# Optimization experiments

Measured on AMD Instinct MI355X. Metric: run time of the kernel, lower is better.

The kernel has to match this reference:

```python
import jax, jax.numpy as jnp
import numpy as np

D_MODEL = 1024
HIDDEN = 4096
NUM_EXPERTS = 8
TOP_K = 2
N_TOKENS = 4 * 2048  # batch * seq


def setup_inputs() -> dict:
    key = jax.random.key(0)
    k_x, k_w, k_i, k1, k2, k3 = jax.random.split(key, 6)
    x = jax.random.normal(k_x, (4, 2048, D_MODEL), dtype=jnp.float32)
    expert_weights = jax.random.uniform(k_w, (N_TOKENS, TOP_K), dtype=jnp.float32)
    expert_indices = jax.random.randint(k_i, (N_TOKENS, TOP_K), 0, NUM_EXPERTS)
    scale = 1.0 / np.sqrt(D_MODEL)
    w1 = jax.random.normal(k1, (NUM_EXPERTS, D_MODEL, HIDDEN), dtype=jnp.float32) * scale
    w3 = jax.random.normal(k3, (NUM_EXPERTS, D_MODEL, HIDDEN), dtype=jnp.float32) * scale
    w2 = jax.random.normal(k2, (NUM_EXPERTS, HIDDEN, D_MODEL), dtype=jnp.float32) * (1.0 / np.sqrt(HIDDEN))
    return {"x": x, "expert_weights": expert_weights, "expert_indices": expert_indices,
            "w1": w1, "w2": w2, "w3": w3}


def reference(x, expert_weights, expert_indices, w1, w2, w3):
    # forward_once of ParallelDroplessMLP (single-rank dropless MoE).
    in_shape = x.shape
    d_model = x.shape[-1]
    num_experts = w1.shape[0]
    xf = x.reshape(-1, d_model)                        # (N, d)
    top_k = expert_weights.shape[-1]
    ew = expert_weights.reshape(-1)                    # (N*top_k,)
    ei = expert_indices.reshape(-1).astype(jnp.int32)  # (N*top_k,)

    # indices_and_bins: stable sort by expert id + histogram
    order = jnp.argsort(ei)                            # (T,) permuted row -> flat (token, k) slot
    tokens_per_expert = jnp.bincount(ei, length=num_experts).astype(jnp.int32)

    # gather: replicate each token top_k times, grouped by expert
    token_of_row = order // top_k                      # (T,)
    xg = jnp.take(xf, token_of_row, axis=0)            # (T, d)

    # grouped GEMM (MegaBlocks-style) SwiGLU per expert via ragged_dot
    h = jax.nn.silu(jax.lax.ragged_dot(xg, w1, tokens_per_expert)) \
        * jax.lax.ragged_dot(xg, w3, tokens_per_expert)            # (T, hidden)
    y = jax.lax.ragged_dot(h, w2, tokens_per_expert)               # (T, d)

    # scatter: weighted un-permute back to token positions
    y = y * ew[order][:, None]
    out = jnp.zeros_like(xf).at[token_of_row].add(y)
    return out.reshape(in_shape), tokens_per_expert
```

## Files before the change

### kernel.cpp

```cpp
#include <hip/hip_runtime.h>

#define NTOK 8192
#define TROWS 16384
#define DM 1024
#define HID 4096
#define NEXP 8
#define MAXT256 72
#define MAXT128 136

typedef __bf16 bf16x8 __attribute__((ext_vector_type(8)));
typedef float  f32x4  __attribute__((ext_vector_type(4)));
typedef short  s16x4  __attribute__((ext_vector_type(4)));

#define BAR() do { asm volatile("" ::: "memory"); __builtin_amdgcn_s_barrier(); asm volatile("" ::: "memory"); } while(0)
#define VM6() asm volatile("s_waitcnt vmcnt(6)" ::: "memory")
#define VM0() asm volatile("s_waitcnt vmcnt(0)" ::: "memory")
#define VM8() asm volatile("s_waitcnt vmcnt(8)" ::: "memory")

__device__ __forceinline__ short f2bf(float f) {
  union { float f; unsigned u; } v; v.f = f;
  unsigned r = (v.u + 0x7fffu + ((v.u >> 16) & 1u)) >> 16;
  return (short)r;
}
__device__ __forceinline__ float bf2f(short s) {
  union { unsigned u; float f; } z; z.u = ((unsigned)(unsigned short)s) << 16; return z.f;
}

__device__ __forceinline__ void gload16(const short* g, short* l) {
  __builtin_amdgcn_global_load_lds(
      (const __attribute__((address_space(1))) void*)g,
      (__attribute__((address_space(3))) void*)l, 16, 0, 0);
}

__global__ void k_meta(const int* __restrict__ ei, int* __restrict__ meta,
                       float* __restrict__ outCounts) {
  __shared__ int c[NEXP];
  int tid = threadIdx.x;
  if (tid < NEXP) c[tid] = 0;
  __syncthreads();
  for (int i = tid; i < TROWS; i += 256) atomicAdd(&c[ei[i]], 1);
  __syncthreads();
  if (tid == 0) {
    int off = 0, s = 0, s2 = 0;
    for (int e = 0; e < NEXP; ++e) {
      int ce = c[e];
      meta[e] = ce;
      meta[8 + e] = off;
      meta[16 + e] = off;
      outCounts[e] = (float)ce;
      for (int r0 = 0; r0 < ce; r0 += 256) {
        meta[32 + 3*s] = e; meta[32 + 3*s + 1] = off + r0;
        meta[32 + 3*s + 2] = (ce - r0 < 256) ? (ce - r0) : 256; ++s;
      }
      for (int r0 = 0; r0 < ce; r0 += 128) {
        meta[256 + 3*s2] = e; meta[256 + 3*s2 + 1] = off + r0;
        meta[256 + 3*s2 + 2] = (ce - r0 < 128) ? (ce - r0) : 128; ++s2;
      }
      off += ce;
    }
    for (; s < MAXT256; ++s)  { meta[32 + 3*s] = 0;  meta[32 + 3*s + 1] = 0;  meta[32 + 3*s + 2] = 0; }
    for (; s2 < MAXT128; ++s2){ meta[256 + 3*s2] = 0; meta[256 + 3*s2 + 1] = 0; meta[256 + 3*s2 + 2] = 0; }
  }
}

__global__ void k_scatter(const int* __restrict__ ei, int* __restrict__ meta,
                          int* __restrict__ rowmap, int* __restrict__ inv) {
  int t = blockIdx.x * blockDim.x + threadIdx.x;
  if (t < TROWS) {
    int e = ei[t];
    int p = atomicAdd(&meta[16 + e], 1);
    rowmap[p] = t;
    inv[t] = p;
  }
}

__global__ void k_transpose64(const float* __restrict__ in, short* __restrict__ out,
                              int R, int C) {
  __shared__ short lt[64][68];
  int e = blockIdx.z;
  int c0 = blockIdx.x * 64, r0 = blockIdx.y * 64;
  int t = threadIdx.x;
  int rr = t >> 4, cc = (t & 15) * 4;
  const float* src = in + ((size_t)e * R + r0 + rr) * C + c0 + cc;
#pragma unroll
  for (int i = 0; i < 4; ++i) {
    f32x4 v = *(const f32x4*)(src + (size_t)i * 16 * C);
#pragma unroll
    for (int j = 0; j < 4; ++j) lt[cc + j][rr + i*16] = f2bf(v[j]);
  }
  __syncthreads();
  int c2 = t >> 4, r4 = (t & 15) * 4;
  short* dst = out + ((size_t)e * C + c0 + c2) * R + r0 + r4;
#pragma unroll
  for (int i = 0; i < 4; ++i) {
    s16x4 o = *(const s16x4*)&lt[c2 + i*16][r4];
    *(s16x4*)(dst + (size_t)i * 16 * R) = o;
  }
}

__global__ void k_cvt_x(const float* __restrict__ x, short* __restrict__ xb) {
  const int n4 = NTOK * DM / 4;
  for (int i = blockIdx.x * blockDim.x + threadIdx.x; i < n4; i += gridDim.x * blockDim.x) {
    f32x4 v = ((const f32x4*)x)[i];
    s16x4 s = { f2bf(v.x), f2bf(v.y), f2bf(v.z), f2bf(v.w) };
    ((s16x4*)xb)[i] = s;
  }
}

__global__ __launch_bounds__(512, 2) void k_gemm1(
    const short* __restrict__ xb, const short* __restrict__ w1t, const short* __restrict__ w3t,
    const int* __restrict__ rowmap, const int* __restrict__ meta, short* __restrict__ hbuf) {
  int bid = blockIdx.x;
  int swz = (bid & 7) * 288 + (bid >> 3);
  int slot = swz % MAXT256;
  int bn   = swz / MAXT256;
  int rows = meta[32 + 3*slot + 2];
  if (rows <= 0) return;
  int e    = meta[32 + 3*slot];
  int row0 = meta[32 + 3*slot + 1];

  __shared__ short lA [2][256 * 64];
  __shared__ short lB1[2][128 * 64];
  __shared__ short lB3[2][128 * 64];

  int tid = threadIdx.x, l = tid & 63, w = tid >> 6;
  int wr = (w >> 2) * 128, wc = (w & 3) * 32;
  int lr = l & 15, cb = (l >> 4) * 16, axor = (lr & 7) << 4;
  int srow = l >> 3;
  int scol = ((l & 7) ^ srow) * 8;

  const short* aG[2][2];
#pragma unroll
  for (int h = 0; h < 2; ++h)
#pragma unroll
    for (int i = 0; i < 2; ++i) {
      int r = h*128 + w*16 + i*8 + srow;
      int rc = r < rows ? r : rows - 1;
      int tok = rowmap[row0 + rc] >> 1;
      aG[h][i] = xb + (size_t)tok * DM + scol;
    }
  const short *b1G[2], *b3G[2];
#pragma unroll
  for (int i = 0; i < 2; ++i) {
    size_t grow = (size_t)e * HID + (size_t)bn * 128 + w*16 + i*8 + srow;
    b1G[i] = w1t + grow * DM + scol;
    b3G[i] = w3t + grow * DM + scol;
  }

  f32x4 acc1[2][4][2], acc3[2][4][2];
#pragma unroll
  for (int h = 0; h < 2; ++h)
#pragma unroll
    for (int i = 0; i < 4; ++i)
#pragma unroll
      for (int j = 0; j < 2; ++j) {
        acc1[h][i][j] = (f32x4){0.f,0.f,0.f,0.f};
        acc3[h][i][j] = (f32x4){0.f,0.f,0.f,0.f};
      }

  auto stgA = [&](int buf, int h, int kt) {
    gload16(aG[h][0] + kt, &lA[buf][(h*128 + w*16    ) * 64]);
    gload16(aG[h][1] + kt, &lA[buf][(h*128 + w*16 + 8) * 64]);
  };
  auto stgB1 = [&](int buf, int kt) {
    gload16(b1G[0] + kt, &lB1[buf][(w*16    ) * 64]);
    gload16(b1G[1] + kt, &lB1[buf][(w*16 + 8) * 64]);
  };
  auto stgB3 = [&](int buf, int kt) {
    gload16(b3G[0] + kt, &lB3[buf][(w*16    ) * 64]);
    gload16(b3G[1] + kt, &lB3[buf][(w*16 + 8) * 64]);
  };

  stgA(0, 0, 0); stgA(0, 1, 0); stgB1(0, 0); stgB3(0, 0);
  stgB1(1, 64); stgB3(1, 64); stgA(1, 0, 64);
  VM6();
  BAR();

  const int NT = DM / 64;
  int c = 0;
  for (int t = 0; t < NT; ++t, c ^= 1) {
    int kn  = t*64 + 64;
    int kn2 = t*64 + 128;
    const char* cA  = (const char*)&lA [c][0];
    const char* cB1 = (const char*)&lB1[c][0];
    const char* cB3 = (const char*)&lB3[c][0];

    bf16x8 alo[4][2], b1w[2][2];
#pragma unroll
    for (int i = 0; i < 4; ++i)
#pragma unroll
      for (int kk = 0; kk < 2; ++kk)
        alo[i][kk] = *(const bf16x8*)(cA + (wr + i*16 + lr)*128 + ((kk*64 + cb) ^ axor));
#pragma unroll
    for (int j = 0; j < 2; ++j)
#pragma unroll
      for (int kk = 0; kk < 2; ++kk)
        b1w[j][kk] = *(const bf16x8*)(cB1 + (wc + j*16 + lr)*128 + ((kk*64 + cb) ^ axor));
    if (t + 1 < NT) stgA(c ^ 1, 1, kn);
    BAR();
    __builtin_amdgcn_s_setprio(1);
#pragma unroll
    for (int i = 0; i < 4; ++i)
#pragma unroll
      for (int j = 0; j < 2; ++j)
#pragma unroll
        for (int kk = 0; kk < 2; ++kk)
          acc1[0][i][j] = __builtin_amdgcn_mfma_f32_16x16x32_bf16(alo[i][kk], b1w[j][kk], acc1[0][i][j], 0, 0, 0);
    __builtin_amdgcn_s_setprio(0);
    BAR();

    bf16x8 b3w[2][2];
#pragma unroll
    for (int j = 0; j < 2; ++j)
#pragma unroll
      for (int kk = 0; kk < 2; ++kk)
        b3w[j][kk] = *(const bf16x8*)(cB3 + (wc + j*16 + lr)*128 + ((kk*64 + cb) ^ axor));
    if (t + 2 < NT) stgB1(c, kn2);
    BAR();
    __builtin_amdgcn_s_setprio(1);
#pragma unroll
    for (int i = 0; i < 4; ++i)
#pragma unroll
      for (int j = 0; j < 2; ++j)
#pragma unroll
        for (int kk = 0; kk < 2; ++kk)
          acc3[0][i][j] = __builtin_amdgcn_mfma_f32_16x16x32_bf16(alo[i][kk], b3w[j][kk], acc3[0][i][j], 0, 0, 0);
    __builtin_amdgcn_s_setprio(0);
    BAR();

    bf16x8 ahi[4][2];
#pragma unroll
    for (int i = 0; i < 4; ++i)
#pragma unroll
      for (int kk = 0; kk < 2; ++kk)
        ahi[i][kk] = *(const bf16x8*)(cA + (wr + 64 + i*16 + lr)*128 + ((kk*64 + cb) ^ axor));
    if (t + 2 < NT) stgB3(c, kn2);
    BAR();
    __builtin_amdgcn_s_setprio(1);
#pragma unroll
    for (int i = 0; i < 4; ++i)
#pragma unroll
      for (int j = 0; j < 2; ++j)
#pragma unroll
        for (int kk = 0; kk < 2; ++kk)
          acc1[1][i][j] = __builtin_amdgcn_mfma_f32_16x16x32_bf16(ahi[i][kk], b1w[j][kk], acc1[1][i][j], 0, 0, 0);
    __builtin_amdgcn_s_setprio(0);
    BAR();

    if (t + 2 < NT) stgA(c, 0, kn2);
    __builtin_amdgcn_s_setprio(1);
#pragma unroll
    for (int i = 0; i < 4; ++i)
#pragma unroll
      for (int j = 0; j < 2; ++j)
#pragma unroll
        for (int kk = 0; kk < 2; ++kk)
          acc3[1][i][j] = __builtin_amdgcn_mfma_f32_16x16x32_bf16(ahi[i][kk], b3w[j][kk], acc3[1][i][j], 0, 0, 0);
    __builtin_amdgcn_s_setprio(0);
    if (t < NT - 2) { VM6(); } else { VM0(); }
    BAR();
  }

#pragma unroll
  for (int h = 0; h < 2; ++h)
#pragma unroll
    for (int i = 0; i < 4; ++i)
#pragma unroll
      for (int q = 0; q < 4; ++q) {
        int r = wr + h*64 + i*16 + (l >> 4)*4 + q;
        if (r < rows) {
          size_t base = (size_t)(row0 + r) * HID + (size_t)bn * 128 + wc;
#pragma unroll
          for (int j = 0; j < 2; ++j) {
            float g = acc1[h][i][j][q], u3 = acc3[h][i][j][q];
            float sv = g / (1.f + __expf(-g));
            hbuf[base + j*16 + lr] = f2bf(sv * u3);
          }
        }
      }
}

__global__ __launch_bounds__(256) void k_gemm2(
    const short* __restrict__ hbuf, const short* __restrict__ w2t,
    const int* __restrict__ meta, short* __restrict__ y) {
  int bid = blockIdx.x;
  int swz = (bid & 7) * (MAXT128 * 8 / 8) + (bid >> 3);
  int slot = swz % MAXT128;
  int bn   = swz / MAXT128;
  int rows = meta[256 + 3*slot + 2];
  if (rows <= 0) return;
  int e    = meta[256 + 3*slot];
  int row0 = meta[256 + 3*slot + 1];

  __shared__ short lA[2][128 * 64];
  __shared__ short lB[2][128 * 64];

  int tid = threadIdx.x;
  int l = tid & 63, w = tid >> 6;

  int srow = w*8 + (l >> 3);
  int scol = ((l & 7) ^ (l >> 3)) * 8;

  const short* aG[4];
  for (int p = 0; p < 4; ++p) {
    int r = p*32 + srow;
    int rc = r < rows ? r : rows - 1;
    aG[p] = hbuf + (size_t)(row0 + rc) * HID + scol;
  }
  const short* bG[4];
  for (int p = 0; p < 4; ++p) {
    size_t grow = (size_t)e * DM + (size_t)bn * 128 + p*32 + srow;
    bG[p] = w2t + grow * HID + scol;
  }

  f32x4 acc[4][4];
  for (int i = 0; i < 4; ++i)
    for (int j = 0; j < 4; ++j) acc[i][j] = (f32x4){0.f, 0.f, 0.f, 0.f};

  int wr = (w >> 1) * 64, wc = (w & 1) * 64;
  int lr = l & 15;
  int cb = (l >> 4) * 16;
  int axor = (lr & 7) << 4;

  auto stage = [&](int buf, int kt) {
#pragma unroll
    for (int p = 0; p < 4; ++p) {
      gload16(aG[p] + kt, &lA[buf][(p*32 + w*8) * 64]);
      gload16(bG[p] + kt, &lB[buf][(p*32 + w*8) * 64]);
    }
  };
  auto compute = [&](int cur) {
    const char* cA = (const char*)&lA[cur][0];
    const char* cB = (const char*)&lB[cur][0];
    __builtin_amdgcn_s_setprio(1);
#pragma unroll
    for (int kk2 = 0; kk2 < 2; ++kk2) {
      int co = (kk2*64 + cb) ^ axor;
      bf16x8 a[4], b[4];
#pragma unroll
      for (int i = 0; i < 4; ++i) a[i] = *(const bf16x8*)(cA + (wr + i*16 + lr)*128 + co);
#pragma unroll
      for (int j = 0; j < 4; ++j) b[j] = *(const bf16x8*)(cB + (wc + j*16 + lr)*128 + co);
#pragma unroll
      for (int i = 0; i < 4; ++i)
#pragma unroll
        for (int j = 0; j < 4; ++j)
          acc[i][j] = __builtin_amdgcn_mfma_f32_16x16x32_bf16(a[i], b[j], acc[i][j], 0, 0, 0);
    }
    __builtin_amdgcn_s_setprio(0);
  };

  stage(0, 0);
  int cur = 0;
  for (int kt = 64; kt <= HID; kt += 64) {
    if (kt < HID) {
      stage(cur ^ 1, kt);
      VM8();
    } else {
      VM0();
    }
    __builtin_amdgcn_s_barrier();
    compute(cur);
    asm volatile("" ::: "memory");
    __builtin_amdgcn_s_barrier();
    cur ^= 1;
  }

  for (int i = 0; i < 4; ++i)
    for (int q = 0; q < 4; ++q) {
      int r = wr + i*16 + (l >> 4)*4 + q;
      if (r < rows) {
        size_t obase = (size_t)(row0 + r) * DM + (size_t)bn * 128 + wc;
        for (int j = 0; j < 4; ++j)
          y[obase + j*16 + lr] = f2bf(acc[i][j][q]);
      }
    }
}

__global__ void k_unperm(const short* __restrict__ y, const int* __restrict__ inv,
                         const float* __restrict__ ew, float* __restrict__ out) {
  int i = blockIdx.x * 256 + threadIdx.x;
  int tok = i >> 8, c = i & 255;
  int p0 = inv[2*tok], p1 = inv[2*tok + 1];
  float w0 = ew[2*tok], w1v = ew[2*tok + 1];
  s16x4 a = ((const s16x4*)y)[(size_t)p0 * 256 + c];
  s16x4 b = ((const s16x4*)y)[(size_t)p1 * 256 + c];
  f32x4 r;
#pragma unroll
  for (int j = 0; j < 4; ++j) r[j] = w0 * bf2f(a[j]) + w1v * bf2f(b[j]);
  ((f32x4*)out)[i] = r;
}

extern "C" void kernel_launch(void* const* d_in, const int* in_sizes, int n_in,
                              void* d_out, int out_size, void* d_ws, size_t ws_size,
                              hipStream_t stream) {
  const float* x  = (const float*)d_in[0];
  const float* ew = (const float*)d_in[1];
  const int*   ei = (const int*)d_in[2];
  const float* w1 = (const float*)d_in[3];
  const float* w2 = (const float*)d_in[4];
  const float* w3 = (const float*)d_in[5];
  float* out = (float*)d_out;
  char*  ws  = (char*)d_ws;

  short* w1t = (short*)(ws + 0);
  short* w3t = (short*)(ws + 67108864);
  short* w2t = (short*)(ws + 134217728);
  short* xb  = (short*)(ws + 201326592);
  short* hb  = (short*)(ws + 218103808);
  int*   meta   = (int*)(ws + 352321536);
  int*   rowmap = (int*)(ws + 352321536 + 8192);
  int*   inv    = (int*)(ws + 352321536 + 73728);
  short* y      = (short*)(ws + 0);

  k_meta<<<1, 256, 0, stream>>>(ei, meta, out + (size_t)NTOK * DM);
  k_scatter<<<TROWS / 256, 256, 0, stream>>>(ei, meta, rowmap, inv);
  k_transpose64<<<dim3(HID/64, DM/64, NEXP), 256, 0, stream>>>(w1, w1t, DM, HID);
  k_transpose64<<<dim3(HID/64, DM/64, NEXP), 256, 0, stream>>>(w3, w3t, DM, HID);
  k_transpose64<<<dim3(DM/64, HID/64, NEXP), 256, 0, stream>>>(w2, w2t, HID, DM);
  k_cvt_x<<<2048, 256, 0, stream>>>(x, xb);
  k_gemm1<<<MAXT256 * (HID/128), 512, 0, stream>>>(xb, w1t, w3t, rowmap, meta, hb);
  k_gemm2<<<MAXT128 * (DM/128), 256, 0, stream>>>(hb, w2t, meta, y);
  k_unperm<<<NTOK * DM / 4 / 256, 256, 0, stream>>>(y, inv, ew, out);
}
```

Before: 801.9 us.

## Software-pipeline gemm2 into quadrant phases with finer-grained LDS prefetch

Restructures the second grouped GEMM's K loop into four quadrant MFMA phases, each issuing a portion of the next tile's global-to-LDS loads and synchronising with barriers, so loads are spread across compute instead of issued in one burst per tile. It also reworks the weight transpose kernel to stage fp32 values in a padded LDS tile and convert to bf16 on the read side. The finer interleaving aims to hide memory latency in gemm2, at the cost of more barriers per K step and more intricate buffer-reuse ordering.

```diff
diff --git a/kernel.cpp b/kernel.cpp
--- a/kernel.cpp
+++ b/kernel.cpp
@@ -15,7 +15,6 @@
 #define BAR() do { asm volatile("" ::: "memory"); __builtin_amdgcn_s_barrier(); asm volatile("" ::: "memory"); } while(0)
 #define VM6() asm volatile("s_waitcnt vmcnt(6)" ::: "memory")
 #define VM0() asm volatile("s_waitcnt vmcnt(0)" ::: "memory")
-#define VM8() asm volatile("s_waitcnt vmcnt(8)" ::: "memory")
 
 __device__ __forceinline__ short f2bf(float f) {
   union { float f; unsigned u; } v; v.f = f;
@@ -76,24 +75,23 @@
 
 __global__ void k_transpose64(const float* __restrict__ in, short* __restrict__ out,
                               int R, int C) {
-  __shared__ short lt[64][68];
+  __shared__ float lt[64][65];
   int e = blockIdx.z;
   int c0 = blockIdx.x * 64, r0 = blockIdx.y * 64;
   int t = threadIdx.x;
   int rr = t >> 4, cc = (t & 15) * 4;
   const float* src = in + ((size_t)e * R + r0 + rr) * C + c0 + cc;
 #pragma unroll
+  for (int i = 0; i < 4; ++i)
+    *(f32x4*)&lt[rr + i*16][cc] = *(const f32x4*)(src + (size_t)i * 16 * C);
+  __syncthreads();
+  int cN = t >> 4, r4 = (t & 15) * 4;
+  short* dst = out + ((size_t)e * C + c0 + cN) * R + r0 + r4;
+#pragma unroll
   for (int i = 0; i < 4; ++i) {
-    f32x4 v = *(const f32x4*)(src + (size_t)i * 16 * C);
-#pragma unroll
-    for (int j = 0; j < 4; ++j) lt[cc + j][rr + i*16] = f2bf(v[j]);
-  }
-  __syncthreads();
-  int c2 = t >> 4, r4 = (t & 15) * 4;
-  short* dst = out + ((size_t)e * C + c0 + c2) * R + r0 + r4;
-#pragma unroll
-  for (int i = 0; i < 4; ++i) {
-    s16x4 o = *(const s16x4*)&lt[c2 + i*16][r4];
+    s16x4 o;
+#pragma unroll
+    for (int j = 0; j < 4; ++j) o[j] = f2bf(lt[r4 + j][cN + i*16]);
     *(s16x4*)(dst + (size_t)i * 16 * R) = o;
   }
 }
@@ -284,7 +282,7 @@
     const short* __restrict__ hbuf, const short* __restrict__ w2t,
     const int* __restrict__ meta, short* __restrict__ y) {
   int bid = blockIdx.x;
-  int swz = (bid & 7) * (MAXT128 * 8 / 8) + (bid >> 3);
+  int swz = (bid & 7) * 136 + (bid >> 3);
   int slot = swz % MAXT128;
   int bn   = swz / MAXT128;
   int rows = meta[256 + 3*slot + 2];
@@ -295,82 +293,138 @@
   __shared__ short lA[2][128 * 64];
   __shared__ short lB[2][128 * 64];
 
-  int tid = threadIdx.x;
-  int l = tid & 63, w = tid >> 6;
-
-  int srow = w*8 + (l >> 3);
-  int scol = ((l & 7) ^ (l >> 3)) * 8;
+  int tid = threadIdx.x, l = tid & 63, w = tid >> 6;
+  int wr = (w >> 1) * 64, wc = (w & 1) * 64;
+  int lr = l & 15, cb = (l >> 4) * 16, axor = (lr & 7) << 4;
+  int srow = l >> 3;
+  int scol = ((l & 7) ^ srow) * 8;
 
   const short* aG[4];
-  for (int p = 0; p < 4; ++p) {
-    int r = p*32 + srow;
+#pragma unroll
+  for (int g = 0; g < 4; ++g) {
+    int r = g*32 + w*8 + srow;
     int rc = r < rows ? r : rows - 1;
-    aG[p] = hbuf + (size_t)(row0 + rc) * HID + scol;
+    aG[g] = hbuf + (size_t)(row0 + rc) * HID + scol;
   }
   const short* bG[4];
-  for (int p = 0; p < 4; ++p) {
-    size_t grow = (size_t)e * DM + (size_t)bn * 128 + p*32 + srow;
-    bG[p] = w2t + grow * HID + scol;
+#pragma unroll
+  for (int g = 0; g < 4; ++g) {
+    size_t grow = (size_t)e * DM + (size_t)bn * 128 + g*32 + w*8 + srow;
+    bG[g] = w2t + grow * HID + scol;
   }
 
   f32x4 acc[4][4];
+#pragma unroll
   for (int i = 0; i < 4; ++i)
-    for (int j = 0; j < 4; ++j) acc[i][j] = (f32x4){0.f, 0.f, 0.f, 0.f};
-
-  int wr = (w >> 1) * 64, wc = (w & 1) * 64;
-  int lr = l & 15;
-  int cb = (l >> 4) * 16;
-  int axor = (lr & 7) << 4;
-
-  auto stage = [&](int buf, int kt) {
-#pragma unroll
-    for (int p = 0; p < 4; ++p) {
-      gload16(aG[p] + kt, &lA[buf][(p*32 + w*8) * 64]);
-      gload16(bG[p] + kt, &lB[buf][(p*32 + w*8) * 64]);
-    }
+#pragma unroll
+    for (int j = 0; j < 4; ++j) acc[i][j] = (f32x4){0.f,0.f,0.f,0.f};
+
+  auto stgA = [&](int buf, int g, int kt) {
+    gload16(aG[g] + kt, &lA[buf][(g*32 + w*8) * 64]);
   };
-  auto compute = [&](int cur) {
-    const char* cA = (const char*)&lA[cur][0];
-    const char* cB = (const char*)&lB[cur][0];
-    __builtin_amdgcn_s_setprio(1);
-#pragma unroll
-    for (int kk2 = 0; kk2 < 2; ++kk2) {
-      int co = (kk2*64 + cb) ^ axor;
-      bf16x8 a[4], b[4];
-#pragma unroll
-      for (int i = 0; i < 4; ++i) a[i] = *(const bf16x8*)(cA + (wr + i*16 + lr)*128 + co);
-#pragma unroll
-      for (int j = 0; j < 4; ++j) b[j] = *(const bf16x8*)(cB + (wc + j*16 + lr)*128 + co);
-#pragma unroll
-      for (int i = 0; i < 4; ++i)
-#pragma unroll
-        for (int j = 0; j < 4; ++j)
-          acc[i][j] = __builtin_amdgcn_mfma_f32_16x16x32_bf16(a[i], b[j], acc[i][j], 0, 0, 0);
-    }
-    __builtin_amdgcn_s_setprio(0);
+  auto stgB = [&](int buf, int g, int kt) {
+    gload16(bG[g] + kt, &lB[buf][(g*32 + w*8) * 64]);
   };
 
-  stage(0, 0);
-  int cur = 0;
-  for (int kt = 64; kt <= HID; kt += 64) {
-    if (kt < HID) {
-      stage(cur ^ 1, kt);
-      VM8();
-    } else {
-      VM0();
-    }
-    __builtin_amdgcn_s_barrier();
-    compute(cur);
-    asm volatile("" ::: "memory");
-    __builtin_amdgcn_s_barrier();
-    cur ^= 1;
-  }
-
+  stgA(0,0,0); stgA(0,1,0); stgA(0,2,0); stgA(0,3,0);
+  stgB(0,0,0); stgB(0,1,0); stgB(0,2,0); stgB(0,3,0);
+  stgB(1,0,64); stgB(1,1,64); stgB(1,2,64); stgB(1,3,64);
+  stgA(1,0,64); stgA(1,1,64);
+  VM6();
+  BAR();
+
+  const int NT = HID / 64;
+  int c = 0;
+  for (int t = 0; t < NT; ++t, c ^= 1) {
+    int kn  = t*64 + 64;
+    int kn2 = t*64 + 128;
+    const char* cA = (const char*)&lA[c][0];
+    const char* cB = (const char*)&lB[c][0];
+
+    bf16x8 alo[2][2], blo[2][2];
+#pragma unroll
+    for (int i = 0; i < 2; ++i)
+#pragma unroll
+      for (int kk = 0; kk < 2; ++kk)
+        alo[i][kk] = *(const bf16x8*)(cA + (wr + i*16 + lr)*128 + ((kk*64 + cb) ^ axor));
+#pragma unroll
+    for (int j = 0; j < 2; ++j)
+#pragma unroll
+      for (int kk = 0; kk < 2; ++kk)
+        blo[j][kk] = *(const bf16x8*)(cB + (wc + j*16 + lr)*128 + ((kk*64 + cb) ^ axor));
+    if (t + 1 < NT) { stgA(c ^ 1, 2, kn); stgA(c ^ 1, 3, kn); }
+    BAR();
+    __builtin_amdgcn_s_setprio(1);
+#pragma unroll
+    for (int i = 0; i < 2; ++i)
+#pragma unroll
+      for (int j = 0; j < 2; ++j)
+#pragma unroll
+        for (int kk = 0; kk < 2; ++kk)
+          acc[i][j] = __builtin_amdgcn_mfma_f32_16x16x32_bf16(alo[i][kk], blo[j][kk], acc[i][j], 0, 0, 0);
+    __builtin_amdgcn_s_setprio(0);
+    BAR();
+
+    bf16x8 bhi[2][2];
+#pragma unroll
+    for (int j = 0; j < 2; ++j)
+#pragma unroll
+      for (int kk = 0; kk < 2; ++kk)
+        bhi[j][kk] = *(const bf16x8*)(cB + (wc + (j+2)*16 + lr)*128 + ((kk*64 + cb) ^ axor));
+    if (t + 2 < NT) { stgB(c, 0, kn2); stgB(c, 1, kn2); }
+    BAR();
+    __builtin_amdgcn_s_setprio(1);
+#pragma unroll
+    for (int i = 0; i < 2; ++i)
+#pragma unroll
+      for (int j = 0; j < 2; ++j)
+#pragma unroll
+        for (int kk = 0; kk < 2; ++kk)
+          acc[i][j+2] = __builtin_amdgcn_mfma_f32_16x16x32_bf16(alo[i][kk], bhi[j][kk], acc[i][j+2], 0, 0, 0);
+    __builtin_amdgcn_s_setprio(0);
+    BAR();
+
+    bf16x8 ahi[2][2];
+#pragma unroll
+    for (int i = 0; i < 2; ++i)
+#pragma unroll
+      for (int kk = 0; kk < 2; ++kk)
+        ahi[i][kk] = *(const bf16x8*)(cA + (wr + (i+2)*16 + lr)*128 + ((kk*64 + cb) ^ axor));
+    if (t + 2 < NT) { stgB(c, 2, kn2); stgB(c, 3, kn2); }
+    BAR();
+    __builtin_amdgcn_s_setprio(1);
+#pragma unroll
+    for (int i = 0; i < 2; ++i)
+#pragma unroll
+      for (int j = 0; j < 2; ++j)
+#pragma unroll
+        for (int kk = 0; kk < 2; ++kk)
+          acc[i+2][j] = __builtin_amdgcn_mfma_f32_16x16x32_bf16(ahi[i][kk], blo[j][kk], acc[i+2][j], 0, 0, 0);
+    __builtin_amdgcn_s_setprio(0);
+    BAR();
+
+    if (t + 2 < NT) { stgA(c, 0, kn2); stgA(c, 1, kn2); }
+    __builtin_amdgcn_s_setprio(1);
+#pragma unroll
+    for (int i = 0; i < 2; ++i)
+#pragma unroll
+      for (int j = 0; j < 2; ++j)
+#pragma unroll
+        for (int kk = 0; kk < 2; ++kk)
+          acc[i+2][j+2] = __builtin_amdgcn_mfma_f32_16x16x32_bf16(ahi[i][kk], bhi[j][kk], acc[i+2][j+2], 0, 0, 0);
+    __builtin_amdgcn_s_setprio(0);
+    if (t < NT - 2) { VM6(); } else { VM0(); }
+    BAR();
+  }
+
+#pragma unroll
   for (int i = 0; i < 4; ++i)
+#pragma unroll
     for (int q = 0; q < 4; ++q) {
       int r = wr + i*16 + (l >> 4)*4 + q;
       if (r < rows) {
         size_t obase = (size_t)(row0 + r) * DM + (size_t)bn * 128 + wc;
+#pragma unroll
         for (int j = 0; j < 4; ++j)
           y[obase + j*16 + lr] = f2bf(acc[i][j][q]);
       }
```

Result: slower. 823.4 us (+2.7%).
